# Kernel tuning notes

Measured on AMD Instinct MI355X. Metric: run time of the kernel, lower is better.

The kernel has to match this reference:

```python
import jax, jax.numpy as jnp
import numpy as np

VOCAB, EMB, H, T = 7000, 256, 512, 5  # char vocab, emb dim, LSTM hidden, num CRF tags


def lstm_scan(x, w_ih, w_hh, b_ih, b_hh, reverse=False):
    # x: [S, B, D]; PyTorch gate order i, f, g, o
    B = x.shape[1]
    Hd = w_hh.shape[1]
    h0 = jnp.zeros((B, Hd), x.dtype)

    def step(carry, xt):
        h, c = carry
        g = xt @ w_ih.T + h @ w_hh.T + (b_ih + b_hh)
        i, f, gg, o = jnp.split(g, 4, axis=-1)
        c = jax.nn.sigmoid(f) * c + jax.nn.sigmoid(i) * jnp.tanh(gg)
        h = jax.nn.sigmoid(o) * jnp.tanh(c)
        return (h, c), h

    _, hs = jax.lax.scan(step, (h0, h0), x, reverse=reverse)
    return hs  # [S, B, H]


def crf_nll_token_mean(em, tags, mask, start, end, trans):
    # em: [S,B,T] float, tags: [S,B] int, mask: [S,B] bool (mask[0] all True)
    S, B, _ = em.shape
    bidx = jnp.arange(B)
    mf = mask.astype(em.dtype)
    # numerator: gold path score
    score = start[tags[0]] + em[0, bidx, tags[0]]

    def num_step(s, x):
        e, tp, t, m = x
        return s + (trans[tp, t] + e[bidx, t]) * m, None

    score, _ = jax.lax.scan(num_step, score, (em[1:], tags[:-1], tags[1:], mf[1:]))
    seq_ends = mask.astype(jnp.int32).sum(0) - 1
    score = score + end[tags[seq_ends, bidx]]
    # denominator: forward algorithm (log partition)
    alpha = start[None, :] + em[0]  # [B,T]

    def den_step(a, x):
        e, m = x
        nxt = jax.nn.logsumexp(a[:, :, None] + trans[None] + e[:, None, :], axis=1)
        return jnp.where(m[:, None], nxt, a), None

    alpha, _ = jax.lax.scan(den_step, alpha, (em[1:], mask[1:]))
    logZ = jax.nn.logsumexp(alpha + end[None, :], axis=-1)
    return -(score - logZ).sum() / mf.sum()  # token_mean NLL


def setup_inputs() -> dict:
    key = jax.random.key(0)
    ks = jax.random.split(key, 24)
    B, S = 64, 512
    text = jax.random.randint(ks[0], (B, S), 1, VOCAB, dtype=jnp.int32)  # no padding -> mask[0] all on
    sbjs = jax.random.randint(ks[1], (B, S), 0, T, dtype=jnp.int32)
    objs = jax.random.randint(ks[2], (B, S), 0, T, dtype=jnp.int32)
    sc = 0.05
    inp = {
        'text': text, 'sbjs': sbjs, 'objs': objs,
        'emb': jax.random.normal(ks[3], (VOCAB, EMB), jnp.float32) * sc,
        'wih_f': jax.random.normal(ks[4], (4 * H, EMB), jnp.float32) * sc,
        'whh_f': jax.random.normal(ks[5], (4 * H, H), jnp.float32) * sc,
        'bih_f': jnp.zeros((4 * H,), jnp.float32),
        'bhh_f': jnp.zeros((4 * H,), jnp.float32),
        'wih_b': jax.random.normal(ks[6], (4 * H, EMB), jnp.float32) * sc,
        'whh_b': jax.random.normal(ks[7], (4 * H, H), jnp.float32) * sc,
        'bih_b': jnp.zeros((4 * H,), jnp.float32),
        'bhh_b': jnp.zeros((4 * H,), jnp.float32),
        'sbj_w': jax.random.normal(ks[8], (T, 2 * H), jnp.float32) * sc,
        'sbj_b': jnp.zeros((T,), jnp.float32),
        'obj_w': jax.random.normal(ks[9], (T, 2 * H), jnp.float32) * sc,
        'obj_b': jnp.zeros((T,), jnp.float32),
        'sbj_start': jax.random.normal(ks[10], (T,), jnp.float32) * sc,
        'sbj_end': jax.random.normal(ks[11], (T,), jnp.float32) * sc,
        'sbj_trans': jax.random.normal(ks[12], (T, T), jnp.float32) * sc,
        'obj_start': jax.random.normal(ks[13], (T,), jnp.float32) * sc,
        'obj_end': jax.random.normal(ks[14], (T,), jnp.float32) * sc,
        'obj_trans': jax.random.normal(ks[15], (T, T), jnp.float32) * sc,
    }
    return inp


def reference(text, sbjs, objs, emb, wih_f, whh_f, bih_f, bhh_f, wih_b, whh_b, bih_b, bhh_b,
              sbj_w, sbj_b, obj_w, obj_b, sbj_start, sbj_end, sbj_trans, obj_start, obj_end, obj_trans):
    mask = (text != 0).T                      # [S,B]
    x = emb[text].transpose(1, 0, 2)          # [S,B,EMB]
    hf = lstm_scan(x, wih_f, whh_f, bih_f, bhh_f, reverse=False)
    hb = lstm_scan(x, wih_b, whh_b, bih_b, bhh_b, reverse=True)
    vec = jnp.concatenate([hf, hb], axis=-1)  # [S,B,2H]
    sbj_feat = vec @ sbj_w.T + sbj_b          # [S,B,T]
    obj_feat = vec @ obj_w.T + obj_b
    loss_sbj = crf_nll_token_mean(sbj_feat, sbjs.T, mask, sbj_start, sbj_end, sbj_trans)
    loss_obj = crf_nll_token_mean(obj_feat, objs.T, mask, obj_start, obj_end, obj_trans)
    loss = 2.0 * (loss_sbj + loss_obj)
    return loss, loss_sbj, loss_obj
```

## Files before the change

### kernel.cpp

```cpp
#include <hip/hip_runtime.h>
#include <hip/hip_bf16.h>

#define S_LEN 512
#define BATCH 64
#define EMB_D 256
#define HID   512
#define NTAG  5

typedef unsigned short u16;
typedef unsigned long long u64;
typedef __attribute__((ext_vector_type(8)))  short bf16x8;
typedef __attribute__((ext_vector_type(16))) float f32x16;

__device__ __forceinline__ float bf2f(u16 u) {
  union { unsigned int i; float f; } v; v.i = ((unsigned int)u) << 16; return v.f;
}
__device__ __forceinline__ u16 f2bf(float f) {
  __hip_bfloat16 h = __float2bfloat16(f);
  union { __hip_bfloat16 h; u16 u; } v; v.h = h; return v.u;
}
__device__ __forceinline__ float sigm(float x) { return 1.0f / (1.0f + __expf(-x)); }
__device__ __forceinline__ float ftanh(float x) {
  float ax = fabsf(x);
  float e  = __expf(-2.0f * ax);
  float t  = (1.0f - e) / (1.0f + e);
  return copysignf(t, x);
}

__device__ __forceinline__ bf16x8 ldg_pin16(const u16* p) {
  float4 r;
  asm volatile("global_load_dwordx4 %0, %1, off" : "=v"(r) : "v"(p));
  return __builtin_bit_cast(bf16x8, r);
}

__global__ void k_prep_w(const float* __restrict__ wihf, const float* __restrict__ whhf,
                         const float* __restrict__ bihf, const float* __restrict__ bhhf,
                         const float* __restrict__ wihb, const float* __restrict__ whhb,
                         const float* __restrict__ bihb, const float* __restrict__ bhhb,
                         u16* __restrict__ Wcat, float* __restrict__ bias)
{
  const int gid = blockIdx.x * blockDim.x + threadIdx.x;
  const int k4  = gid % 192;
  const int rem = gid / 192;
  const int row = rem & 2047;
  const int d   = rem >> 11;
  const float* wih = d ? wihb : wihf;
  const float* whh = d ? whhb : whhf;
  const int k = k4 * 4;
  float4 v;
  if (k < EMB_D) v = *(const float4*)(wih + (size_t)row * EMB_D + k);
  else           v = *(const float4*)(whh + (size_t)row * HID + (k - EMB_D));
  union { u16 u[4]; uint2 q; } pk;
  pk.u[0] = f2bf(v.x); pk.u[1] = f2bf(v.y); pk.u[2] = f2bf(v.z); pk.u[3] = f2bf(v.w);
  *(uint2*)(Wcat + ((size_t)(d * 2048 + row)) * 768 + k) = pk.q;
  if (gid < 4096) {
    const int dd = gid >> 11, r = gid & 2047;
    bias[gid] = dd ? (bihb[r] + bhhb[r]) : (bihf[r] + bhhf[r]);
  }
}

__global__ void k_embed(const int* __restrict__ text, const float* __restrict__ emb,
                        u16* __restrict__ xz)
{
  const int gid = blockIdx.x * blockDim.x + threadIdx.x;
  const int e4 = gid & 63;
  const int sb = gid >> 6;
  const int b  = sb & 63;
  const int s  = sb >> 6;
  const int row = text[b * S_LEN + s];
  float4 v = *(const float4*)(emb + (size_t)row * EMB_D + e4 * 4);
  union { u16 u[4]; uint2 q; } pk;
  pk.u[0] = f2bf(v.x); pk.u[1] = f2bf(v.y); pk.u[2] = f2bf(v.z); pk.u[3] = f2bf(v.w);
  *(uint2*)(xz + ((size_t)(s * BATCH + b)) * EMB_D + e4 * 4) = pk.q;
}

__launch_bounds__(256, 1)
__global__ void k_lstm(const u16* __restrict__ Wcat, const float* __restrict__ bias,
                       const u16* __restrict__ xz, u16* __restrict__ hbuf,
                       int* __restrict__ cnt)
{
  const int bid  = blockIdx.x;
  const int d    = bid >> 5;
  const int k0   = (bid & 31) * 16;
  const int tid  = threadIdx.x;
  const int w    = tid >> 6;
  const int lane = tid & 63;
  const int rt   = w >> 1, nt = w & 1;
  const int ln31 = lane & 31, lhi = lane >> 5;
  const int hbase = k0 + rt * 8;
  const int bcol  = nt * 32 + ln31;

  bf16x8 af[48];
  {
    const int m    = ln31;
    const int grow = (m >> 3) * HID + hbase + (m & 7);
    const u16* wr  = Wcat + ((size_t)(d * 2048 + grow)) * 768 + lhi * 8;
    #pragma unroll
    for (int ks = 0; ks < 48; ++ks) af[ks] = ldg_pin16(wr + ks * 16);
  }
  asm volatile("s_waitcnt vmcnt(0)" ::: "memory");
  __builtin_amdgcn_sched_barrier(0);

  float bsv[16];
  #pragma unroll
  for (int q = 0; q < 4; ++q)
    #pragma unroll
    for (int i = 0; i < 4; ++i)
      bsv[q * 4 + i] = bias[d * 2048 + q * HID + hbase + 4 * lhi + i];
  float cst[4] = {0.f, 0.f, 0.f, 0.f};

  for (int it = 0; it < S_LEN; ++it) {
    const int t = d ? (S_LEN - 1 - it) : it;

    f32x16 acc;
    #pragma unroll
    for (int r = 0; r < 16; ++r) acc[r] = bsv[r];

    {
      const u16* xb = xz + ((size_t)t * BATCH + bcol) * EMB_D + lhi * 8;
      #pragma unroll
      for (int c = 0; c < 16; ++c) {
        bf16x8 xf = *(const bf16x8*)(xb + c * 16);
        acc = __builtin_amdgcn_mfma_f32_32x32x16_bf16(af[c], xf, acc, 0, 0, 0);
      }
    }

    if (it > 0) {
      if (tid == 0) {
        const int* flg = cnt + (size_t)(d * S_LEN + it - 1) * 16;
        while (__hip_atomic_load(flg, __ATOMIC_RELAXED, __HIP_MEMORY_SCOPE_AGENT) < 32)
          __builtin_amdgcn_s_sleep(1);
        __builtin_amdgcn_fence(__ATOMIC_ACQUIRE, "agent");
      }
      __syncthreads();

      const int tprev = d ? (t + 1) : (t - 1);
      const u16* hb = hbuf + (((size_t)d * S_LEN + tprev) * BATCH + bcol) * HID + lhi * 8;
      #pragma unroll
      for (int c = 0; c < 32; ++c) {
        bf16x8 hf = *(const bf16x8*)(hb + c * 16);
        acc = __builtin_amdgcn_mfma_f32_32x32x16_bf16(af[16 + c], hf, acc, 0, 0, 0);
      }
    }

    u16 hu[4];
    #pragma unroll
    for (int i = 0; i < 4; ++i) {
      const float gi = acc[i], gf = acc[4 + i], gg = acc[8 + i], go = acc[12 + i];
      const float ig = sigm(gi), fg = sigm(gf), g2 = ftanh(gg), og = sigm(go);
      cst[i] = fg * cst[i] + ig * g2;
      hu[i] = f2bf(og * ftanh(cst[i]));
    }
    const u64 pk = (u64)hu[0] | ((u64)hu[1] << 16) | ((u64)hu[2] << 32) | ((u64)hu[3] << 48);
    *(u64*)(hbuf + (((size_t)d * S_LEN + t) * BATCH + bcol) * HID + hbase + 4 * lhi) = pk;

    __syncthreads();
    if (tid == 0) {
      __builtin_amdgcn_fence(__ATOMIC_RELEASE, "agent");
      __hip_atomic_fetch_add(cnt + (size_t)(d * S_LEN + it) * 16, 1,
                             __ATOMIC_RELAXED, __HIP_MEMORY_SCOPE_AGENT);
    }
  }
}

__global__ void k_heads(const u16* __restrict__ hbuf,
                        const float* __restrict__ sbj_w, const float* __restrict__ sbj_b,
                        const float* __restrict__ obj_w, const float* __restrict__ obj_b,
                        float* __restrict__ em_s, float* __restrict__ em_o)
{
  const int wid  = blockIdx.x * 4 + (threadIdx.x >> 6);
  const int lane = threadIdx.x & 63;
  if (wid >= S_LEN * BATCH) return;
  const int s = wid >> 6, b = wid & 63;
  const int dsel = lane >> 5;
  const int off  = (lane * 16) & 511;
  const u16* src = hbuf + (((size_t)dsel * S_LEN + s) * BATCH + b) * HID + off;
  uint4 p0 = *(const uint4*)(src);
  uint4 p1 = *(const uint4*)(src + 8);
  unsigned int pw[8] = { p0.x, p0.y, p0.z, p0.w, p1.x, p1.y, p1.z, p1.w };
  float z[16];
  #pragma unroll
  for (int i = 0; i < 8; ++i) {
    z[2 * i]     = bf2f((u16)(pw[i] & 0xffffu));
    z[2 * i + 1] = bf2f((u16)(pw[i] >> 16));
  }
  #pragma unroll
  for (int r = 0; r < 10; ++r) {
    const float* wr = (r < 5) ? (sbj_w + r * (2 * HID)) : (obj_w + (r - 5) * (2 * HID));
    float p = 0.f;
    #pragma unroll
    for (int m4 = 0; m4 < 4; ++m4) {
      float4 w4 = *(const float4*)(wr + lane * 16 + m4 * 4);
      p += w4.x * z[m4*4] + w4.y * z[m4*4+1] + w4.z * z[m4*4+2] + w4.w * z[m4*4+3];
    }
    #pragma unroll
    for (int offs = 32; offs; offs >>= 1) p += __shfl_down(p, offs);
    if (lane == 0) {
      if (r < 5) em_s[(size_t)wid * NTAG + r]       = p + sbj_b[r];
      else       em_o[(size_t)wid * NTAG + (r - 5)] = p + obj_b[r - 5];
    }
  }
}

__global__ void k_crf(const float* __restrict__ em_s, const float* __restrict__ em_o,
                      const int* __restrict__ sbjs, const int* __restrict__ objs,
                      const int* __restrict__ text,
                      const float* __restrict__ s_st, const float* __restrict__ s_en,
                      const float* __restrict__ s_tr,
                      const float* __restrict__ o_st, const float* __restrict__ o_en,
                      const float* __restrict__ o_tr,
                      float* __restrict__ perb, float* __restrict__ cntb)
{
  const int c = blockIdx.x & 1;
  const int b = blockIdx.x >> 1;
  const int j = threadIdx.x;

  const float* em    = c ? em_o : em_s;
  const int*   tags  = c ? objs : sbjs;
  const float* start = c ? o_st : s_st;
  const float* endv  = c ? o_en : s_en;
  const float* trans = c ? o_tr : s_tr;

  float num = 0.f, cnt = 0.f;
  for (int s = j; s < S_LEN; s += 64) {
    const int m = (text[b * S_LEN + s] != 0) ? 1 : 0;
    cnt += (float)m;
    const int tg = tags[b * S_LEN + s];
    if (s == 0) {
      num += start[tg] + em[(size_t)b * NTAG + tg];
    } else if (m) {
      const int tp = tags[b * S_LEN + s - 1];
      num += trans[tp * NTAG + tg] + em[((size_t)s * BATCH + b) * NTAG + tg];
    }
  }
  #pragma unroll
  for (int off = 32; off; off >>= 1) { num += __shfl_down(num, off); cnt += __shfl_down(cnt, off); }
  num = __shfl(num, 0); cnt = __shfl(cnt, 0);
  const int seq_end = (int)cnt - 1;
  if (j == 0) num += endv[tags[b * S_LEN + seq_end]];

  float tr0 = 0, tr1 = 0, tr2 = 0, tr3 = 0, tr4 = 0, st = 0, en = 0;
  if (j < NTAG) {
    tr0 = trans[0 * NTAG + j]; tr1 = trans[1 * NTAG + j]; tr2 = trans[2 * NTAG + j];
    tr3 = trans[3 * NTAG + j]; tr4 = trans[4 * NTAG + j];
    st = start[j]; en = endv[j];
  }
  float alpha = (j < NTAG) ? (st + em[(size_t)b * NTAG + j]) : -1e30f;
  for (int s = 1; s < S_LEN; ++s) {
    const float a0 = __shfl(alpha, 0), a1 = __shfl(alpha, 1), a2 = __shfl(alpha, 2),
                a3 = __shfl(alpha, 3), a4 = __shfl(alpha, 4);
    const int m = (text[b * S_LEN + s] != 0);
    if (j < NTAG) {
      const float v0 = a0 + tr0, v1 = a1 + tr1, v2 = a2 + tr2, v3 = a3 + tr3, v4 = a4 + tr4;
      float mx = fmaxf(fmaxf(fmaxf(v0, v1), fmaxf(v2, v3)), v4);
      float sm = expf(v0 - mx) + expf(v1 - mx) + expf(v2 - mx) + expf(v3 - mx) + expf(v4 - mx);
      float nxt = mx + logf(sm) + em[((size_t)s * BATCH + b) * NTAG + j];
      if (m) alpha = nxt;
    }
  }
  float v  = (j < NTAG) ? (alpha + en) : -1e30f;
  float mx = v;
  #pragma unroll
  for (int off = 1; off < 8; off <<= 1) mx = fmaxf(mx, __shfl_xor(mx, off));
  float ex = (j < NTAG) ? expf(v - mx) : 0.f;
  #pragma unroll
  for (int off = 1; off < 8; off <<= 1) ex += __shfl_xor(ex, off);
  if (j == 0) {
    perb[c * BATCH + b] = num - (mx + logf(ex));
    cntb[c * BATCH + b] = cnt;
  }
}

__global__ void k_final(const float* __restrict__ perb, const float* __restrict__ cntb,
                        float* __restrict__ out)
{
  if (threadIdx.x == 0 && blockIdx.x == 0) {
    float s0 = 0, c0 = 0, s1 = 0, c1 = 0;
    for (int b = 0; b < BATCH; ++b) {
      s0 += perb[b];         c0 += cntb[b];
      s1 += perb[BATCH + b]; c1 += cntb[BATCH + b];
    }
    const float ls = -s0 / c0, lo = -s1 / c1;
    out[0] = 2.f * (ls + lo);
    out[1] = ls;
    out[2] = lo;
  }
}

extern "C" void kernel_launch(void* const* d_in, const int* in_sizes, int n_in,
                              void* d_out, int out_size, void* d_ws, size_t ws_size,
                              hipStream_t stream)
{
  const int*   text  = (const int*)d_in[0];
  const int*   sbjs  = (const int*)d_in[1];
  const int*   objs  = (const int*)d_in[2];
  const float* emb   = (const float*)d_in[3];
  const float* wih_f = (const float*)d_in[4];
  const float* whh_f = (const float*)d_in[5];
  const float* bih_f = (const float*)d_in[6];
  const float* bhh_f = (const float*)d_in[7];
  const float* wih_b = (const float*)d_in[8];
  const float* whh_b = (const float*)d_in[9];
  const float* bih_b = (const float*)d_in[10];
  const float* bhh_b = (const float*)d_in[11];
  const float* sbj_w = (const float*)d_in[12];
  const float* sbj_b = (const float*)d_in[13];
  const float* obj_w = (const float*)d_in[14];
  const float* obj_b = (const float*)d_in[15];
  const float* s_st  = (const float*)d_in[16];
  const float* s_en  = (const float*)d_in[17];
  const float* s_tr  = (const float*)d_in[18];
  const float* o_st  = (const float*)d_in[19];
  const float* o_en  = (const float*)d_in[20];
  const float* o_tr  = (const float*)d_in[21];

  char* w = (char*)d_ws;
  u16*   Wcat = (u16*)(w + 0);
  float* bias = (float*)(w + 6291456);
  u16*   xz   = (u16*)(w + 6307840);
  u16*   hbuf = (u16*)(w + 23085056);
  float* em_s = (float*)(w + 90193920);
  float* em_o = (float*)(w + 90849280);
  float* perb = (float*)(w + 91504640);
  float* cntb = (float*)(w + 91505152);
  int*   cnt  = (int*)(w + 91505664);

  hipMemsetAsync(cnt, 0, 2 * S_LEN * 16 * sizeof(int), stream);

  k_prep_w<<<3072, 256, 0, stream>>>(wih_f, whh_f, bih_f, bhh_f,
                                     wih_b, whh_b, bih_b, bhh_b, Wcat, bias);
  k_embed<<<8192, 256, 0, stream>>>(text, emb, xz);

  void* args[] = { (void*)&Wcat, (void*)&bias, (void*)&xz, (void*)&hbuf, (void*)&cnt };
  hipLaunchCooperativeKernel((const void*)k_lstm, dim3(64), dim3(256), args, 0, stream);

  k_heads<<<8192, 256, 0, stream>>>(hbuf, sbj_w, sbj_b, obj_w, obj_b, em_s, em_o);
  k_crf<<<128, 64, 0, stream>>>(em_s, em_o, sbjs, objs, text,
                                s_st, s_en, s_tr, o_st, o_en, o_tr, perb, cntb);
  k_final<<<1, 1, 0, stream>>>(perb, cntb, (float*)d_out);
}
```

Baseline: 4.992 ms.

## Split MFMA accumulator chains and replace agent fences with atomic h loads/stores

```diff
diff --git a/kernel.cpp b/kernel.cpp
--- a/kernel.cpp
+++ b/kernel.cpp
@@ -112,16 +112,17 @@
   for (int it = 0; it < S_LEN; ++it) {
     const int t = d ? (S_LEN - 1 - it) : it;
 
-    f32x16 acc;
-    #pragma unroll
-    for (int r = 0; r < 16; ++r) acc[r] = bsv[r];
+    f32x16 acc0, acc1;
+    #pragma unroll
+    for (int r = 0; r < 16; ++r) { acc0[r] = bsv[r]; acc1[r] = 0.f; }
 
     {
       const u16* xb = xz + ((size_t)t * BATCH + bcol) * EMB_D + lhi * 8;
       #pragma unroll
       for (int c = 0; c < 16; ++c) {
         bf16x8 xf = *(const bf16x8*)(xb + c * 16);
-        acc = __builtin_amdgcn_mfma_f32_32x32x16_bf16(af[c], xf, acc, 0, 0, 0);
+        if (c & 1) acc1 = __builtin_amdgcn_mfma_f32_32x32x16_bf16(af[c], xf, acc1, 0, 0, 0);
+        else       acc0 = __builtin_amdgcn_mfma_f32_32x32x16_bf16(af[c], xf, acc0, 0, 0, 0);
       }
     }
 
@@ -130,33 +131,42 @@
         const int* flg = cnt + (size_t)(d * S_LEN + it - 1) * 16;
         while (__hip_atomic_load(flg, __ATOMIC_RELAXED, __HIP_MEMORY_SCOPE_AGENT) < 32)
           __builtin_amdgcn_s_sleep(1);
-        __builtin_amdgcn_fence(__ATOMIC_ACQUIRE, "agent");
       }
+      __builtin_amdgcn_fence(__ATOMIC_ACQUIRE, "workgroup");
       __syncthreads();
 
       const int tprev = d ? (t + 1) : (t - 1);
-      const u16* hb = hbuf + (((size_t)d * S_LEN + tprev) * BATCH + bcol) * HID + lhi * 8;
+      const u64* hb = (const u64*)(hbuf + (((size_t)d * S_LEN + tprev) * BATCH + bcol) * HID);
       #pragma unroll
       for (int c = 0; c < 32; ++c) {
-        bf16x8 hf = *(const bf16x8*)(hb + c * 16);
-        acc = __builtin_amdgcn_mfma_f32_32x32x16_bf16(af[16 + c], hf, acc, 0, 0, 0);
+        union { u64 q[2]; bf16x8 v; } hf;
+        hf.q[0] = __hip_atomic_load(hb + c * 4 + lhi * 2,
+                                    __ATOMIC_RELAXED, __HIP_MEMORY_SCOPE_AGENT);
+        hf.q[1] = __hip_atomic_load(hb + c * 4 + lhi * 2 + 1,
+                                    __ATOMIC_RELAXED, __HIP_MEMORY_SCOPE_AGENT);
+        if (c & 1) acc1 = __builtin_amdgcn_mfma_f32_32x32x16_bf16(af[16 + c], hf.v, acc1, 0, 0, 0);
+        else       acc0 = __builtin_amdgcn_mfma_f32_32x32x16_bf16(af[16 + c], hf.v, acc0, 0, 0, 0);
       }
     }
 
     u16 hu[4];
     #pragma unroll
     for (int i = 0; i < 4; ++i) {
-      const float gi = acc[i], gf = acc[4 + i], gg = acc[8 + i], go = acc[12 + i];
+      const float gi = acc0[i]      + acc1[i];
+      const float gf = acc0[4 + i]  + acc1[4 + i];
+      const float gg = acc0[8 + i]  + acc1[8 + i];
+      const float go = acc0[12 + i] + acc1[12 + i];
       const float ig = sigm(gi), fg = sigm(gf), g2 = ftanh(gg), og = sigm(go);
       cst[i] = fg * cst[i] + ig * g2;
       hu[i] = f2bf(og * ftanh(cst[i]));
     }
     const u64 pk = (u64)hu[0] | ((u64)hu[1] << 16) | ((u64)hu[2] << 32) | ((u64)hu[3] << 48);
-    *(u64*)(hbuf + (((size_t)d * S_LEN + t) * BATCH + bcol) * HID + hbase + 4 * lhi) = pk;
+    u64* hw = (u64*)(hbuf + (((size_t)d * S_LEN + t) * BATCH + bcol) * HID + hbase + 4 * lhi);
+    __hip_atomic_store(hw, pk, __ATOMIC_RELAXED, __HIP_MEMORY_SCOPE_AGENT);
 
     __syncthreads();
     if (tid == 0) {
-      __builtin_amdgcn_fence(__ATOMIC_RELEASE, "agent");
+      asm volatile("s_waitcnt vmcnt(0)" ::: "memory");
       __hip_atomic_fetch_add(cnt + (size_t)(d * S_LEN + it) * 16, 1,
                              __ATOMIC_RELAXED, __HIP_MEMORY_SCOPE_AGENT);
     }
```

After: 6.150 ms. 1.23x slower.
